# Optimization experiments

Hardware: AMD Instinct MI355X
Metric: run time of the kernel (lower is better)

The kernel has to match this reference:

```python
import jax, jax.numpy as jnp
import numpy as np

N_USER, N_TX, E = 50000, 50000, 600000
D_USER, D_TX, D_ALIGN, HID, OUT = 128, 64, 128, 256, 128


def setup_inputs() -> dict:
    key = jax.random.key(0)
    ks = jax.random.split(key, 16)
    s = 0.05
    return {
        "x_user": jax.random.normal(ks[0], (N_USER, D_USER), jnp.float32),
        "x_tx": jax.random.normal(ks[1], (N_TX, D_TX), jnp.float32),
        "edge_user_tx": jax.random.randint(ks[2], (2, E), 0, N_USER),
        "edge_tx_user": jax.random.randint(ks[3], (2, E), 0, N_TX),
        "W_align_user": jax.random.normal(ks[4], (D_USER, D_ALIGN), jnp.float32) * s,
        "b_align_user": jnp.zeros((D_ALIGN,), jnp.float32),
        "W_align_tx": jax.random.normal(ks[5], (D_TX, D_ALIGN), jnp.float32) * s,
        "b_align_tx": jnp.zeros((D_ALIGN,), jnp.float32),
        "eps_ut": jnp.zeros((), jnp.float32),
        "eps_tu": jnp.zeros((), jnp.float32),
        "W1_ut": jax.random.normal(ks[6], (D_TX + D_ALIGN, HID), jnp.float32) * s,
        "b1_ut": jnp.zeros((HID,), jnp.float32),
        "W2_ut": jax.random.normal(ks[7], (HID, OUT), jnp.float32) * s,
        "b2_ut": jnp.zeros((OUT,), jnp.float32),
        "W1_tu": jax.random.normal(ks[8], (D_USER + D_ALIGN, HID), jnp.float32) * s,
        "b1_tu": jnp.zeros((HID,), jnp.float32),
        "W2_tu": jax.random.normal(ks[9], (HID, OUT), jnp.float32) * s,
        "b2_tu": jnp.zeros((OUT,), jnp.float32),
    }


def _mlp(h, W1, b1, W2, b2):
    return jnp.maximum(h @ W1 + b1, 0.0) @ W2 + b2


def _hexgin_conv(x_src, x_dst, edge_index, W_a, b_a, eps, W1, b1, W2, b2):
    # align src features, gather along edges, scatter-sum into dst nodes
    a_src = x_src @ W_a + b_a                       # [N_src, D_ALIGN]
    msgs = a_src[edge_index[0]]                     # [E, D_ALIGN] gather
    agg = jax.ops.segment_sum(msgs, edge_index[1], num_segments=x_dst.shape[0])
    h = jnp.concatenate([(1.0 + eps) * x_dst, agg], axis=1)
    return _mlp(h, W1, b1, W2, b2)


def reference(x_user, x_tx, edge_user_tx, edge_tx_user,
              W_align_user, b_align_user, W_align_tx, b_align_tx,
              eps_ut, eps_tu,
              W1_ut, b1_ut, W2_ut, b2_ut,
              W1_tu, b1_tu, W2_tu, b2_tu):
    # relation (user, makes, tx): updates tx nodes
    out_tx = _hexgin_conv(x_user, x_tx, edge_user_tx,
                          W_align_user, b_align_user, eps_ut,
                          W1_ut, b1_ut, W2_ut, b2_ut)
    # relation (tx, to, user): updates user nodes
    out_user = _hexgin_conv(x_tx, x_user, edge_tx_user,
                            W_align_tx, b_align_tx, eps_tu,
                            W1_tu, b1_tu, W2_tu, b2_tu)
    # HeteroConv aggr='sum': single relation per target, so plain outputs
    return out_user, out_tx
```

## Files before the change

### kernel.cpp

```cpp
#include <hip/hip_runtime.h>
#include <hip/hip_bf16.h>


#define D_USER 128
#define D_TX 64
#define D_ALIGN 128
#define HID 256
#define OUT_D 128
#define NNODE 50000
#define BI 32
#define MAXSLOT 62
#define HPAD 264

typedef __attribute__((ext_vector_type(8))) short short8;
typedef __attribute__((ext_vector_type(4))) float f32x4;
typedef unsigned short ush;

__device__ __forceinline__ ush f2bf(float f) {
    union { float f; unsigned u; } v; v.f = f;
    unsigned u = v.u + 0x7fffu + ((v.u >> 16) & 1u);
    return (ush)(u >> 16);
}
__device__ __forceinline__ float2 bfu2f(unsigned u) {
    union { unsigned u; float f; } a, b;
    a.u = (u & 0xffffu) << 16;
    b.u = u & 0xffff0000u;
    return make_float2(a.f, b.f);
}
__device__ __forceinline__ unsigned f2bfu(float2 v) {
    return (unsigned)f2bf(v.x) | ((unsigned)f2bf(v.y) << 16);
}
__device__ __forceinline__ uint4 scale_bf8(uint4 v, float e) {
    unsigned* w = (unsigned*)&v;
    #pragma unroll
    for (int t = 0; t < 4; ++t) {
        float2 f = bfu2f(w[t]);
        w[t] = f2bfu(make_float2(f.x * e, f.y * e));
    }
    return v;
}


__device__ __forceinline__ void dev_fill(const int* __restrict__ e, int E, int i,
                                         int* __restrict__ pad, int dbase)
{
    int d = dbase + e[E + i];
    int s = e[i];
    int pos = atomicAdd(&pad[(size_t)d * BI], 1);
    if (pos < MAXSLOT)
        ((ush*)pad)[(size_t)d * (2 * BI) + 2 + pos] = (ush)s;
}

__device__ __forceinline__ void dev_prep(int b, int tid,
    const float* __restrict__ xu, ush* __restrict__ xbu,
    const float* __restrict__ xt, ush* __restrict__ xbt, int n8u, int n8t,
    const float* __restrict__ Wa_u, const float* __restrict__ ba_u,
    const float* __restrict__ W1_ut,
    const float* __restrict__ Wa_t, const float* __restrict__ ba_t,
    const float* __restrict__ W1_tu,
    const float* __restrict__ W2_ut, const float* __restrict__ W2_tu,
    ush* __restrict__ Bt1a, float* __restrict__ bfv1,
    ush* __restrict__ Bt1b, float* __restrict__ bfv2,
    ush* __restrict__ Bt2a, ush* __restrict__ Bt2b, int gb)
{
    if (b < gb) {
        int i = b * 256 + tid;
        const float* x; ush* xb; int j;
        if (i < n8u) { x = xu; xb = xbu; j = i; }
        else if (i < n8u + n8t) { x = xt; xb = xbt; j = i - n8u; }
        else return;
        const float4 a = *reinterpret_cast<const float4*>(&x[(size_t)j * 8]);
        const float4 c = *reinterpret_cast<const float4*>(&x[(size_t)j * 8 + 4]);
        ush o[8];
        o[0] = f2bf(a.x); o[1] = f2bf(a.y); o[2] = f2bf(a.z); o[3] = f2bf(a.w);
        o[4] = f2bf(c.x); o[5] = f2bf(c.y); o[6] = f2bf(c.z); o[7] = f2bf(c.w);
        *reinterpret_cast<uint4*>(&xb[(size_t)j * 8]) = *reinterpret_cast<uint4*>(o);
        return;
    }
    int idx = (b - gb) * 256 + tid;
    const int KT = 192;
    const int SEG1 = HID * (KT + 1);
    const int SEG2 = OUT_D * HID;
    if (idx < 2 * SEG1) {
        bool r2 = idx >= SEG1;
        int id = r2 ? idx - SEG1 : idx;
        const float* Wa = r2 ? Wa_t : Wa_u;
        const float* ba = r2 ? ba_t : ba_u;
        const float* W1 = r2 ? W1_tu : W1_ut;
        ush* Bt = r2 ? Bt1b : Bt1a;
        float* bfv = r2 ? bfv2 : bfv1;
        const int Dd = r2 ? 128 : 64;
        int c = id & (HID - 1);
        int k = id >> 8;
        const float* w1bot = W1 + (size_t)Dd * HID;
        if (k < Dd) {
            Bt[(size_t)c * KT + k] = f2bf(W1[(size_t)k * HID + c]);
        } else if (k < KT) {
            int ks = k - Dd;
            float acc = 0.f;
            for (int j = 0; j < D_ALIGN; ++j)
                acc += Wa[ks * D_ALIGN + j] * w1bot[(size_t)j * HID + c];
            Bt[(size_t)c * KT + k] = f2bf(acc);
        } else {
            float acc = 0.f;
            for (int j = 0; j < D_ALIGN; ++j)
                acc += ba[j] * w1bot[(size_t)j * HID + c];
            bfv[c] = acc;
        }
    } else if (idx < 2 * SEG1 + 2 * SEG2) {
        int id = idx - 2 * SEG1;
        bool r2 = id >= SEG2;
        if (r2) id -= SEG2;
        const float* W2 = r2 ? W2_tu : W2_ut;
        ush* Bt2 = r2 ? Bt2b : Bt2a;
        int c = id & (OUT_D - 1);
        int k = id >> 7;
        Bt2[(size_t)c * HID + k] = f2bf(W2[(size_t)k * OUT_D + c]);
    }
}

__device__ __forceinline__ int slot_word(const int* blk, int lane)
{
    return ((lane & 31) < 31) ? blk[1 + (lane & 31)] : 0;
}
__device__ __forceinline__ int slot_get(int word, int j)
{
    return (j & 1) ? ((word >> 16) & 0xffff) : (word & 0xffff);
}

__device__ __forceinline__ void dev_agg128(int w, int lane,
    const ush* __restrict__ xbu, const int* __restrict__ pad, ush* __restrict__ Sb1)
{
    const int* blk = pad + (size_t)w * BI;
    const int n = min(blk[0], MAXSLOT);
    const int word = slot_word(blk, lane);
    float2 acc = make_float2(0.f, 0.f);
    int i = 0;
    for (; i + 4 <= n; i += 4) {
        int wa = __shfl(word, i >> 1);
        int wb = __shfl(word, (i >> 1) + 1);
        int s0 = wa & 0xffff, s1 = (wa >> 16) & 0xffff;
        int s2 = wb & 0xffff, s3 = (wb >> 16) & 0xffff;
        unsigned v0 = *reinterpret_cast<const unsigned*>(&xbu[(size_t)s0 * 128 + 2 * lane]);
        unsigned v1 = *reinterpret_cast<const unsigned*>(&xbu[(size_t)s1 * 128 + 2 * lane]);
        unsigned v2 = *reinterpret_cast<const unsigned*>(&xbu[(size_t)s2 * 128 + 2 * lane]);
        unsigned v3 = *reinterpret_cast<const unsigned*>(&xbu[(size_t)s3 * 128 + 2 * lane]);
        float2 f0 = bfu2f(v0), f1 = bfu2f(v1), f2 = bfu2f(v2), f3 = bfu2f(v3);
        acc.x += (f0.x + f1.x) + (f2.x + f3.x);
        acc.y += (f0.y + f1.y) + (f2.y + f3.y);
    }
    for (; i < n; ++i) {
        int ww = __shfl(word, i >> 1);
        int s0 = slot_get(ww, i);
        unsigned v0 = *reinterpret_cast<const unsigned*>(&xbu[(size_t)s0 * 128 + 2 * lane]);
        float2 f0 = bfu2f(v0);
        acc.x += f0.x; acc.y += f0.y;
    }
    *reinterpret_cast<unsigned*>(&Sb1[(size_t)w * 128 + 2 * lane]) = f2bfu(acc);
}

__device__ __forceinline__ void dev_agg64(int w2, int lane,
    const ush* __restrict__ xbt, const int* __restrict__ pad, ush* __restrict__ Sb2)
{
    const int* blk = pad + (size_t)(NNODE + w2) * BI;
    const int n = min(blk[0], MAXSLOT);
    const int word = slot_word(blk, lane);
    const int half = lane >> 5, l2 = lane & 31;
    float2 acc = make_float2(0.f, 0.f);
    int i = 0;
    for (; i + 4 <= n; i += 4) {
        int ja = i + half, jb = i + 2 + half;
        int wa = __shfl(word, ja >> 1);
        int wb = __shfl(word, jb >> 1);
        int s0 = slot_get(wa, ja), s1 = slot_get(wb, jb);
        unsigned v0 = *reinterpret_cast<const unsigned*>(&xbt[(size_t)s0 * 64 + 2 * l2]);
        unsigned v1 = *reinterpret_cast<const unsigned*>(&xbt[(size_t)s1 * 64 + 2 * l2]);
        float2 f0 = bfu2f(v0), f1 = bfu2f(v1);
        acc.x += f0.x + f1.x;
        acc.y += f0.y + f1.y;
    }
    for (; i + 2 <= n; i += 2) {
        int j = i + half;
        int ww = __shfl(word, j >> 1);
        int s0 = slot_get(ww, j);
        unsigned v0 = *reinterpret_cast<const unsigned*>(&xbt[(size_t)s0 * 64 + 2 * l2]);
        float2 f0 = bfu2f(v0);
        acc.x += f0.x; acc.y += f0.y;
    }
    if (i < n && half == 0) {
        int ww = __shfl(word, i >> 1);
        int s0 = slot_get(ww, i);
        unsigned v0 = *reinterpret_cast<const unsigned*>(&xbt[(size_t)s0 * 64 + 2 * l2]);
        float2 f0 = bfu2f(v0);
        acc.x += f0.x; acc.y += f0.y;
    }
    acc.x += __shfl_xor(acc.x, 32);
    acc.y += __shfl_xor(acc.y, 32);
    if (half == 0)
        *reinterpret_cast<unsigned*>(&Sb2[(size_t)w2 * 64 + 2 * l2]) = f2bfu(acc);
}


__global__ __launch_bounds__(256) void kA(
    const int* __restrict__ e_ut, int E, int* __restrict__ pad,
    const float* __restrict__ xu, ush* __restrict__ xbu,
    const float* __restrict__ xt, ush* __restrict__ xbt, int n8u, int n8t,
    const float* __restrict__ Wa_u, const float* __restrict__ ba_u,
    const float* __restrict__ W1_ut,
    const float* __restrict__ Wa_t, const float* __restrict__ ba_t,
    const float* __restrict__ W1_tu,
    const float* __restrict__ W2_ut, const float* __restrict__ W2_tu,
    ush* __restrict__ Bt1a, float* __restrict__ bfv1,
    ush* __restrict__ Bt1b, float* __restrict__ bfv2,
    ush* __restrict__ Bt2a, ush* __restrict__ Bt2b, int gf, int gb)
{
    int b = blockIdx.x, tid = threadIdx.x;
    if (b < gf) {
        int i = b * 256 + tid;
        if (i < E) dev_fill(e_ut, E, i, pad, 0);
    } else {
        dev_prep(b - gf, tid, xu, xbu, xt, xbt, n8u, n8t,
                 Wa_u, ba_u, W1_ut, Wa_t, ba_t, W1_tu, W2_ut, W2_tu,
                 Bt1a, bfv1, Bt1b, bfv2, Bt2a, Bt2b, gb);
    }
}

__global__ __launch_bounds__(256) void kB(
    const int* __restrict__ e_tu, int E, int* __restrict__ pad,
    const ush* __restrict__ xbu, ush* __restrict__ Sb1, int gf)
{
    int b = blockIdx.x, tid = threadIdx.x;
    if (b < gf) {
        int i = b * 256 + tid;
        if (i < E) dev_fill(e_tu, E, i, pad, NNODE);
    } else {
        int w = (b - gf) * 4 + (tid >> 6);
        if (w < NNODE) dev_agg128(w, tid & 63, xbu, pad, Sb1);
    }
}

__global__ __launch_bounds__(256) void kC(
    const ush* __restrict__ xbt, const int* __restrict__ pad, ush* __restrict__ Sb2)
{
    int w2 = blockIdx.x * 4 + (threadIdx.x >> 6);
    if (w2 < NNODE) dev_agg64(w2, threadIdx.x & 63, xbt, pad, Sb2);
}

__global__ __launch_bounds__(256) void mlpF(
    const ush* __restrict__ xbt, const ush* __restrict__ xbu,
    const ush* __restrict__ Sb1, const ush* __restrict__ Sb2,
    const ush* __restrict__ Bt1a, const ush* __restrict__ Bt1b,
    const float* __restrict__ bfv1, const float* __restrict__ bfv2,
    const float* __restrict__ b1_ut, const float* __restrict__ b1_tu,
    const ush* __restrict__ Bt2a, const ush* __restrict__ Bt2b,
    const float* __restrict__ b2_ut, const float* __restrict__ b2_tu,
    const int* __restrict__ pad,
    const float* __restrict__ eps_ut, const float* __restrict__ eps_tu,
    float* __restrict__ out_tx, float* __restrict__ out_user, int M)
{
    __shared__ ush Hs[64 * HPAD];

    const int tid = threadIdx.x;
    const bool r2 = blockIdx.y != 0;
    const int bm = blockIdx.x * 64;
    const ush* xdst = r2 ? xbu : xbt;
    const int Dd = r2 ? 128 : 64;
    const ush* Sb = r2 ? Sb2 : Sb1;
    const int Dsrc = r2 ? 64 : 128;
    const ush* Bt1 = r2 ? Bt1b : Bt1a;
    const float* bfv = r2 ? bfv2 : bfv1;
    const float* b1 = r2 ? b1_tu : b1_ut;
    const ush* Bt2 = r2 ? Bt2b : Bt2a;
    const float* b2 = r2 ? b2_tu : b2_ut;
    const int* dgp = pad + (size_t)(r2 ? NNODE : 0) * BI;
    float* out = r2 ? out_user : out_tx;
    const float e = 1.f + (r2 ? eps_tu[0] : eps_ut[0]);

    const int lane = tid & 63, wn = tid >> 6;
    const int lo = lane & 15, hi = lane >> 4;

    f32x4 acc[4][4];
    #pragma unroll
    for (int a = 0; a < 4; ++a)
        #pragma unroll
        for (int b = 0; b < 4; ++b)
            acc[a][b] = f32x4{0.f, 0.f, 0.f, 0.f};

    const int KT1 = 192;
    for (int k0 = 0; k0 < KT1; k0 += 32) {
        const ush* src; int ld; int kb; bool sc;
        if (k0 < Dd) { src = xdst; ld = Dd; kb = k0; sc = true; }
        else         { src = Sb;   ld = Dsrc; kb = k0 - Dd; sc = false; }
        short8 bv[4];
        #pragma unroll
        for (int fj = 0; fj < 4; ++fj) {
            int row = min(bm + fj * 16 + lo, M - 1);
            uint4 v = *reinterpret_cast<const uint4*>(&src[(size_t)row * ld + kb + hi * 8]);
            if (sc) v = scale_bf8(v, e);
            bv[fj] = *reinterpret_cast<short8*>(&v);
        }
        short8 av[4];
        #pragma unroll
        for (int fi = 0; fi < 4; ++fi)
            av[fi] = *reinterpret_cast<const short8*>(
                &Bt1[(size_t)(wn * 64 + fi * 16 + lo) * KT1 + k0 + hi * 8]);
        #pragma unroll
        for (int fi = 0; fi < 4; ++fi)
            #pragma unroll
            for (int fj = 0; fj < 4; ++fj)
                acc[fi][fj] = __builtin_amdgcn_mfma_f32_16x16x32_bf16(av[fi], bv[fj], acc[fi][fj], 0, 0, 0);
    }

    #pragma unroll
    for (int fi = 0; fi < 4; ++fi) {
        int colb = wn * 64 + fi * 16 + hi * 4;
        float4 b1v = *reinterpret_cast<const float4*>(&b1[colb]);
        float4 bfl = *reinterpret_cast<const float4*>(&bfv[colb]);
        #pragma unroll
        for (int fj = 0; fj < 4; ++fj) {
            int r = fj * 16 + lo;
            int gr = bm + r;
            float dgv = (gr < M) ? (float)dgp[(size_t)gr * BI] : 0.f;
            float v0 = fmaxf(acc[fi][fj][0] + b1v.x + dgv * bfl.x, 0.f);
            float v1 = fmaxf(acc[fi][fj][1] + b1v.y + dgv * bfl.y, 0.f);
            float v2 = fmaxf(acc[fi][fj][2] + b1v.z + dgv * bfl.z, 0.f);
            float v3 = fmaxf(acc[fi][fj][3] + b1v.w + dgv * bfl.w, 0.f);
            uint2 u;
            u.x = f2bfu(make_float2(v0, v1));
            u.y = f2bfu(make_float2(v2, v3));
            *reinterpret_cast<uint2*>(&Hs[r * HPAD + colb]) = u;
        }
    }

    __syncthreads();

    f32x4 acc2[2][4];
    #pragma unroll
    for (int a = 0; a < 2; ++a)
        #pragma unroll
        for (int b = 0; b < 4; ++b)
            acc2[a][b] = f32x4{0.f, 0.f, 0.f, 0.f};

    for (int k0 = 0; k0 < HID; k0 += 32) {
        short8 av2[2], bv2[4];
        #pragma unroll
        for (int fi = 0; fi < 2; ++fi)
            av2[fi] = *reinterpret_cast<const short8*>(
                &Bt2[(size_t)(wn * 32 + fi * 16 + lo) * HID + k0 + hi * 8]);
        #pragma unroll
        for (int fj = 0; fj < 4; ++fj)
            bv2[fj] = *reinterpret_cast<const short8*>(&Hs[(fj * 16 + lo) * HPAD + k0 + hi * 8]);
        #pragma unroll
        for (int fi = 0; fi < 2; ++fi)
            #pragma unroll
            for (int fj = 0; fj < 4; ++fj)
                acc2[fi][fj] = __builtin_amdgcn_mfma_f32_16x16x32_bf16(av2[fi], bv2[fj], acc2[fi][fj], 0, 0, 0);
    }

    #pragma unroll
    for (int fi = 0; fi < 2; ++fi) {
        int colb = wn * 32 + fi * 16 + hi * 4;
        float4 b2v = *reinterpret_cast<const float4*>(&b2[colb]);
        #pragma unroll
        for (int fj = 0; fj < 4; ++fj) {
            int gr = bm + fj * 16 + lo;
            if (gr >= M) continue;
            float4 o;
            o.x = acc2[fi][fj][0] + b2v.x;
            o.y = acc2[fi][fj][1] + b2v.y;
            o.z = acc2[fi][fj][2] + b2v.z;
            o.w = acc2[fi][fj][3] + b2v.w;
            *reinterpret_cast<float4*>(&out[(size_t)gr * OUT_D + colb]) = o;
        }
    }
}

extern "C" void kernel_launch(void* const* d_in, const int* in_sizes, int n_in,
                              void* d_out, int out_size, void* d_ws, size_t ws_size,
                              hipStream_t stream)
{
    const float* x_user   = (const float*)d_in[0];
    const float* x_tx     = (const float*)d_in[1];
    const int*   e_ut     = (const int*)d_in[2];
    const int*   e_tu     = (const int*)d_in[3];
    const float* Wa_user  = (const float*)d_in[4];
    const float* ba_user  = (const float*)d_in[5];
    const float* Wa_tx    = (const float*)d_in[6];
    const float* ba_tx    = (const float*)d_in[7];
    const float* eps_ut   = (const float*)d_in[8];
    const float* eps_tu   = (const float*)d_in[9];
    const float* W1_ut    = (const float*)d_in[10];
    const float* b1_ut    = (const float*)d_in[11];
    const float* W2_ut    = (const float*)d_in[12];
    const float* b2_ut    = (const float*)d_in[13];
    const float* W1_tu    = (const float*)d_in[14];
    const float* b1_tu    = (const float*)d_in[15];
    const float* W2_tu    = (const float*)d_in[16];
    const float* b2_tu    = (const float*)d_in[17];

    const int N_user = in_sizes[0] / D_USER;
    const int N_tx   = in_sizes[1] / D_TX;
    const int E      = in_sizes[2] / 2;
    const int NT     = 2 * NNODE;

    float* out_user = (float*)d_out;
    float* out_tx   = (float*)d_out + (size_t)N_user * OUT_D;

    int*   pad   = (int*)d_ws;
    float* fws   = (float*)d_ws;
    ush*   Bt1a  = (ush*)(fws + 3300000);
    ush*   Bt1b  = (ush*)(fws + 3330000);
    ush*   Bt2a  = (ush*)(fws + 3360000);
    ush*   Bt2b  = (ush*)(fws + 3380000);
    float* bfv1  = fws + 3400000;
    float* bfv2  = fws + 3401000;
    ush*   xbu   = (ush*)(fws + 3410000);
    ush*   xbt   = (ush*)(fws + 6700000);
    ush*   Sb1   = (ush*)(fws + 8400000);
    ush*   Sb2   = (ush*)(fws + 11700000);

    const int threads = 256;
    const int n8u = N_user * D_USER / 8, n8t = N_tx * D_TX / 8;
    const int gf  = (E + 255) / 256;
    const int gb  = (n8u + n8t + 255) / 256;
    const int gw  = (2 * HID * 193 + 2 * OUT_D * HID + 255) / 256;
    const int ga  = (NNODE + 3) / 4;
    const int nbF = (NNODE + 63) / 64;

    hipMemsetAsync(pad, 0, (size_t)NT * BI * sizeof(int), stream);

    kA<<<gf + gb + gw, threads, 0, stream>>>(
        e_ut, E, pad, x_user, xbu, x_tx, xbt, n8u, n8t,
        Wa_user, ba_user, W1_ut, Wa_tx, ba_tx, W1_tu, W2_ut, W2_tu,
        Bt1a, bfv1, Bt1b, bfv2, Bt2a, Bt2b, gf, gb);

    kB<<<gf + ga, threads, 0, stream>>>(e_tu, E, pad, xbu, Sb1, gf);

    kC<<<ga, threads, 0, stream>>>(xbt, pad, Sb2);

    dim3 gF(nbF, 2);
    mlpF<<<gF, threads, 0, stream>>>(
        xbt, xbu, Sb1, Sb2, Bt1a, Bt1b, bfv1, bfv2, b1_ut, b1_tu,
        Bt2a, Bt2b, b2_ut, b2_tu, pad, eps_ut, eps_tu,
        out_tx, out_user, NNODE);
}
```

Measured before the change: 204.7 us.

## Stage MLP activations and both weight matrices in LDS with coalesced loads

The fused MLP kernel now copies its whole 64x192 input tile and the full W1 (256x192) into shared memory with coalesced 16-byte loads up front. It then runs the first GEMM from LDS instead of doing strided per-fragment global loads. W2 is also staged into LDS before the second GEMM. The LDS footprint grows to about 125 KB per block, which likely limits occupancy to one block per CU, and latency hiding now depends on that single block.

Result: no change. 201.0 us (-1.8%).

```diff
diff --git a/kernel.cpp b/kernel.cpp
--- a/kernel.cpp
+++ b/kernel.cpp
@@ -10,7 +10,6 @@
 #define NNODE 50000
 #define BI 32
 #define MAXSLOT 62
-#define HPAD 264
 
 typedef __attribute__((ext_vector_type(8))) short short8;
 typedef __attribute__((ext_vector_type(4))) float f32x4;
@@ -258,7 +257,7 @@
     const float* __restrict__ eps_ut, const float* __restrict__ eps_tu,
     float* __restrict__ out_tx, float* __restrict__ out_user, int M)
 {
-    __shared__ ush Hs[64 * HPAD];
+    __shared__ ush lds[64000];
 
     const int tid = threadIdx.x;
     const bool r2 = blockIdx.y != 0;
@@ -278,6 +277,31 @@
 
     const int lane = tid & 63, wn = tid >> 6;
     const int lo = lane & 15, hi = lane >> 4;
+    const int KT1 = 192;
+
+    const int sA_r = tid >> 2, sA_c8 = tid & 3;
+    const int sB_c0 = tid >> 2, sB_ku = tid & 3;
+
+    #pragma unroll
+    for (int k = 0; k < 6; ++k) {
+        const int k0 = k * 32;
+        const ush* src; int ld, kb; bool sc;
+        if (k0 < Dd) { src = xdst; ld = Dd; kb = k0; sc = true; }
+        else         { src = Sb;   ld = Dsrc; kb = k0 - Dd; sc = false; }
+        int gr = bm + sA_r;
+        uint4 va = uint4{0u, 0u, 0u, 0u};
+        if (gr < M)
+            va = *reinterpret_cast<const uint4*>(&src[(size_t)gr * ld + kb + sA_c8 * 8]);
+        if (sc) va = scale_bf8(va, e);
+        *reinterpret_cast<uint4*>(&lds[sA_r * 200 + k0 + sA_c8 * 8]) = va;
+        #pragma unroll
+        for (int q = 0; q < 4; ++q) {
+            int c = sB_c0 + 64 * q;
+            uint4 v = *reinterpret_cast<const uint4*>(&Bt1[(size_t)c * KT1 + k0 + sB_ku * 8]);
+            *reinterpret_cast<uint4*>(&lds[12800 + c * 200 + k0 + sB_ku * 8]) = v;
+        }
+    }
+    __syncthreads();
 
     f32x4 acc[4][4];
     #pragma unroll
@@ -286,30 +310,24 @@
         for (int b = 0; b < 4; ++b)
             acc[a][b] = f32x4{0.f, 0.f, 0.f, 0.f};
 
-    const int KT1 = 192;
-    for (int k0 = 0; k0 < KT1; k0 += 32) {
-        const ush* src; int ld; int kb; bool sc;
-        if (k0 < Dd) { src = xdst; ld = Dd; kb = k0; sc = true; }
-        else         { src = Sb;   ld = Dsrc; kb = k0 - Dd; sc = false; }
-        short8 bv[4];
-        #pragma unroll
-        for (int fj = 0; fj < 4; ++fj) {
-            int row = min(bm + fj * 16 + lo, M - 1);
-            uint4 v = *reinterpret_cast<const uint4*>(&src[(size_t)row * ld + kb + hi * 8]);
-            if (sc) v = scale_bf8(v, e);
-            bv[fj] = *reinterpret_cast<short8*>(&v);
-        }
-        short8 av[4];
+    #pragma unroll
+    for (int k = 0; k < 6; ++k) {
+        short8 av[4], bv[4];
         #pragma unroll
         for (int fi = 0; fi < 4; ++fi)
             av[fi] = *reinterpret_cast<const short8*>(
-                &Bt1[(size_t)(wn * 64 + fi * 16 + lo) * KT1 + k0 + hi * 8]);
+                &lds[12800 + (wn * 64 + fi * 16 + lo) * 200 + k * 32 + hi * 8]);
+        #pragma unroll
+        for (int fj = 0; fj < 4; ++fj)
+            bv[fj] = *reinterpret_cast<const short8*>(
+                &lds[(fj * 16 + lo) * 200 + k * 32 + hi * 8]);
         #pragma unroll
         for (int fi = 0; fi < 4; ++fi)
             #pragma unroll
             for (int fj = 0; fj < 4; ++fj)
                 acc[fi][fj] = __builtin_amdgcn_mfma_f32_16x16x32_bf16(av[fi], bv[fj], acc[fi][fj], 0, 0, 0);
     }
+    __syncthreads();
 
     #pragma unroll
     for (int fi = 0; fi < 4; ++fi) {
@@ -328,10 +346,18 @@
             uint2 u;
             u.x = f2bfu(make_float2(v0, v1));
             u.y = f2bfu(make_float2(v2, v3));
-            *reinterpret_cast<uint2*>(&Hs[r * HPAD + colb]) = u;
+            *reinterpret_cast<uint2*>(&lds[r * 264 + colb]) = u;
         }
     }
-
+    #pragma unroll
+    for (int k = 0; k < 8; ++k) {
+        #pragma unroll
+        for (int q = 0; q < 2; ++q) {
+            int c = sB_c0 + 64 * q;
+            uint4 v = *reinterpret_cast<const uint4*>(&Bt2[(size_t)c * HID + k * 32 + sB_ku * 8]);
+            *reinterpret_cast<uint4*>(&lds[16896 + c * 264 + k * 32 + sB_ku * 8]) = v;
+        }
+    }
     __syncthreads();
 
     f32x4 acc2[2][4];
@@ -341,15 +367,17 @@
         for (int b = 0; b < 4; ++b)
             acc2[a][b] = f32x4{0.f, 0.f, 0.f, 0.f};
 
-    for (int k0 = 0; k0 < HID; k0 += 32) {
+    #pragma unroll
+    for (int k = 0; k < 8; ++k) {
         short8 av2[2], bv2[4];
         #pragma unroll
         for (int fi = 0; fi < 2; ++fi)
             av2[fi] = *reinterpret_cast<const short8*>(
-                &Bt2[(size_t)(wn * 32 + fi * 16 + lo) * HID + k0 + hi * 8]);
+                &lds[16896 + (wn * 32 + fi * 16 + lo) * 264 + k * 32 + hi * 8]);
         #pragma unroll
         for (int fj = 0; fj < 4; ++fj)
-            bv2[fj] = *reinterpret_cast<const short8*>(&Hs[(fj * 16 + lo) * HPAD + k0 + hi * 8]);
+            bv2[fj] = *reinterpret_cast<const short8*>(
+                &lds[(fj * 16 + lo) * 264 + k * 32 + hi * 8]);
         #pragma unroll
         for (int fi = 0; fi < 2; ++fi)
             #pragma unroll
```
